# Kernel tuning notes

Measured on AMD Instinct MI355X. Metric: run time of the kernel, lower is better.

The kernel has to match this reference:

```python
import jax, jax.numpy as jnp
import numpy as np


def setup_inputs() -> dict:
    key = jax.random.key(0)
    k1, k2, k3 = jax.random.split(key, 3)
    B, L = 128, 4096           # batch, max document length
    O, W = 10, 5               # max options, max words per option
    V = 50000                  # vocab size for word indices
    document_indices = jax.random.randint(k1, (B, L), 0, V, dtype=jnp.int64)
    document_probabilities = jax.random.uniform(k2, (B, L), dtype=jnp.float32)
    options = jax.random.randint(k3, (B, O, W), 0, V, dtype=jnp.int64)
    return {
        "document_indices": document_indices,
        "document_probabilities": document_probabilities,
        "options": options,
    }


def reference(document_indices, document_probabilities, options):
    # match: (B, O, W, L) -- True where an option word equals a document word
    match = options[:, :, :, None] == document_indices[:, None, None, :]
    # per option-word probability: sum doc probabilities at matching positions
    word_probs = jnp.sum(
        jnp.where(match, document_probabilities[:, None, None, :], jnp.float32(0.0)),
        axis=3,
    )  # (B, O, W)
    sum_option_words = jnp.sum(word_probs, axis=2)  # (B, O)
    # multiword_option_mode == 'mean': divide by number of non-padding words
    divisor = jnp.sum((options != 0).astype(jnp.float32), axis=2)  # (B, O)
    return sum_option_words / divisor
```

## Files before the change

### kernel.cpp

```cpp
#include <hip/hip_runtime.h>

#define BB 128
#define LL 4096
#define OO 10
#define WW 5

__global__ __launch_bounds__(256) void OptionAttentionSum_kernel(
    const int* __restrict__ doc_idx,
    const float* __restrict__ doc_prob,
    const int* __restrict__ options,
    float* __restrict__ out)
{
    const int bo = blockIdx.x;
    const int b = bo / OO;
    const int t = threadIdx.x;

    const int* opt = options + bo * WW;
    const int w0 = opt[0], w1 = opt[1], w2 = opt[2], w3 = opt[3], w4 = opt[4];

    const int4*   idx4 = (const int4*)(doc_idx + (long)b * LL);
    const float4* p4   = (const float4*)(doc_prob + (long)b * LL);

    float acc = 0.0f;
#pragma unroll
    for (int it = 0; it < 4; ++it) {
        const int i = it * 256 + t;
        const int4   d = idx4[i];
        const float4 p = p4[i];
        acc += p.x * (float)((d.x == w0) + (d.x == w1) + (d.x == w2) + (d.x == w3) + (d.x == w4));
        acc += p.y * (float)((d.y == w0) + (d.y == w1) + (d.y == w2) + (d.y == w3) + (d.y == w4));
        acc += p.z * (float)((d.z == w0) + (d.z == w1) + (d.z == w2) + (d.z == w3) + (d.z == w4));
        acc += p.w * (float)((d.w == w0) + (d.w == w1) + (d.w == w2) + (d.w == w3) + (d.w == w4));
    }

#pragma unroll
    for (int off = 32; off > 0; off >>= 1)
        acc += __shfl_down(acc, off, 64);

    __shared__ float warp_sums[4];
    const int wave = t >> 6;
    const int lane = t & 63;
    if (lane == 0) warp_sums[wave] = acc;
    __syncthreads();

    if (t == 0) {
        const float total = warp_sums[0] + warp_sums[1] + warp_sums[2] + warp_sums[3];
        const float divisor = (float)((w0 != 0) + (w1 != 0) + (w2 != 0) + (w3 != 0) + (w4 != 0));
        out[bo] = total / divisor;
    }
}

extern "C" void kernel_launch(void* const* d_in, const int* in_sizes, int n_in,
                              void* d_out, int out_size, void* d_ws, size_t ws_size,
                              hipStream_t stream) {
    const int*   doc_idx  = (const int*)d_in[0];
    const float* doc_prob = (const float*)d_in[1];
    const int*   options  = (const int*)d_in[2];
    float*       out      = (float*)d_out;

    OptionAttentionSum_kernel<<<BB * OO, 256, 0, stream>>>(doc_idx, doc_prob, options, out);
}
```

Before: 64.46 us.

## Process all options per batch row in one block to reuse document loads

Each block now handles one batch row with 1024 threads, loading each document element once and testing it against all 10 options' 50 words, keeping 10 accumulators per thread. This removes the 10x redundant reads of the document indices and probabilities that the per-option blocks caused. In exchange, only 128 blocks are launched, so parallelism drops, register pressure rises, and there are ten wave reductions per block. Indexing w[0]+t*WW with a runtime t may push the word array into scratch memory.

```diff
diff --git a/kernel.cpp b/kernel.cpp
--- a/kernel.cpp
+++ b/kernel.cpp
@@ -5,48 +5,61 @@
 #define OO 10
 #define WW 5
 
-__global__ __launch_bounds__(256) void OptionAttentionSum_kernel(
+__global__ __launch_bounds__(1024) void OptionAttentionSum_kernel(
     const int* __restrict__ doc_idx,
     const float* __restrict__ doc_prob,
     const int* __restrict__ options,
     float* __restrict__ out)
 {
-    const int bo = blockIdx.x;
-    const int b = bo / OO;
+    const int b = blockIdx.x;
     const int t = threadIdx.x;
 
-    const int* opt = options + bo * WW;
-    const int w0 = opt[0], w1 = opt[1], w2 = opt[2], w3 = opt[3], w4 = opt[4];
+    const int* opt = options + b * (OO * WW);
+    int w[OO][WW];
+#pragma unroll
+    for (int o = 0; o < OO; ++o)
+#pragma unroll
+        for (int k = 0; k < WW; ++k)
+            w[o][k] = opt[o * WW + k];
 
-    const int4*   idx4 = (const int4*)(doc_idx + (long)b * LL);
-    const float4* p4   = (const float4*)(doc_prob + (long)b * LL);
+    const int4   d = ((const int4*)(doc_idx + (long)b * LL))[t];
+    const float4 p = ((const float4*)(doc_prob + (long)b * LL))[t];
 
-    float acc = 0.0f;
+    float acc[OO];
 #pragma unroll
-    for (int it = 0; it < 4; ++it) {
-        const int i = it * 256 + t;
-        const int4   d = idx4[i];
-        const float4 p = p4[i];
-        acc += p.x * (float)((d.x == w0) + (d.x == w1) + (d.x == w2) + (d.x == w3) + (d.x == w4));
-        acc += p.y * (float)((d.y == w0) + (d.y == w1) + (d.y == w2) + (d.y == w3) + (d.y == w4));
-        acc += p.z * (float)((d.z == w0) + (d.z == w1) + (d.z == w2) + (d.z == w3) + (d.z == w4));
-        acc += p.w * (float)((d.w == w0) + (d.w == w1) + (d.w == w2) + (d.w == w3) + (d.w == w4));
+    for (int o = 0; o < OO; ++o) acc[o] = 0.0f;
+
+#pragma unroll
+    for (int o = 0; o < OO; ++o) {
+        acc[o] += p.x * (float)((d.x == w[o][0]) + (d.x == w[o][1]) + (d.x == w[o][2]) + (d.x == w[o][3]) + (d.x == w[o][4]));
+        acc[o] += p.y * (float)((d.y == w[o][0]) + (d.y == w[o][1]) + (d.y == w[o][2]) + (d.y == w[o][3]) + (d.y == w[o][4]));
+        acc[o] += p.z * (float)((d.z == w[o][0]) + (d.z == w[o][1]) + (d.z == w[o][2]) + (d.z == w[o][3]) + (d.z == w[o][4]));
+        acc[o] += p.w * (float)((d.w == w[o][0]) + (d.w == w[o][1]) + (d.w == w[o][2]) + (d.w == w[o][3]) + (d.w == w[o][4]));
     }
 
 #pragma unroll
-    for (int off = 32; off > 0; off >>= 1)
-        acc += __shfl_down(acc, off, 64);
+    for (int o = 0; o < OO; ++o)
+#pragma unroll
+        for (int off = 32; off > 0; off >>= 1)
+            acc[o] += __shfl_down(acc[o], off, 64);
 
-    __shared__ float warp_sums[4];
+    __shared__ float wsum[16][OO];
     const int wave = t >> 6;
     const int lane = t & 63;
-    if (lane == 0) warp_sums[wave] = acc;
+    if (lane == 0) {
+#pragma unroll
+        for (int o = 0; o < OO; ++o) wsum[wave][o] = acc[o];
+    }
     __syncthreads();
 
-    if (t == 0) {
-        const float total = warp_sums[0] + warp_sums[1] + warp_sums[2] + warp_sums[3];
-        const float divisor = (float)((w0 != 0) + (w1 != 0) + (w2 != 0) + (w3 != 0) + (w4 != 0));
-        out[bo] = total / divisor;
+    if (t < OO) {
+        float total = 0.0f;
+#pragma unroll
+        for (int v = 0; v < 16; ++v) total += wsum[v][t];
+        const int* ow = w[0] + t * WW;
+        const float divisor = (float)((ow[0] != 0) + (ow[1] != 0) + (ow[2] != 0) +
+                                      (ow[3] != 0) + (ow[4] != 0));
+        out[b * OO + t] = total / divisor;
     }
 }
 
@@ -58,5 +71,5 @@
     const int*   options  = (const int*)d_in[2];
     float*       out      = (float*)d_out;
 
-    OptionAttentionSum_kernel<<<BB * OO, 256, 0, stream>>>(doc_idx, doc_prob, options, out);
+    OptionAttentionSum_kernel<<<BB, 1024, 0, stream>>>(doc_idx, doc_prob, options, out);
 }
```

Measured after the change: 67.66 us. 1.05x slower.

## Process two options per block to halve document reloads

Applied to the files above, without the earlier changes.

Each block now handles two options of the same batch row, so the document indices and probabilities are loaded once and compared against ten words instead of five. The grid shrinks from 1280 to 640 blocks, and blocks are ordered batch-minor so that neighbouring blocks read different documents. This cuts redundant global/L2 traffic, at the cost of less parallelism and more ALU work per thread.

```diff
diff --git a/kernel.cpp b/kernel.cpp
--- a/kernel.cpp
+++ b/kernel.cpp
@@ -11,42 +11,53 @@
     const int* __restrict__ options,
     float* __restrict__ out)
 {
-    const int bo = blockIdx.x;
-    const int b = bo / OO;
+    const int b    = blockIdx.x & (BB - 1);
+    const int pair = blockIdx.x >> 7;
+    const int o0 = pair * 2, o1 = pair * 2 + 1;
     const int t = threadIdx.x;
 
-    const int* opt = options + bo * WW;
-    const int w0 = opt[0], w1 = opt[1], w2 = opt[2], w3 = opt[3], w4 = opt[4];
+    const int* opt = options + (b * OO + o0) * WW;
+    const int a0 = opt[0], a1 = opt[1], a2 = opt[2], a3 = opt[3], a4 = opt[4];
+    const int b0 = opt[5], b1 = opt[6], b2 = opt[7], b3 = opt[8], b4 = opt[9];
 
     const int4*   idx4 = (const int4*)(doc_idx + (long)b * LL);
     const float4* p4   = (const float4*)(doc_prob + (long)b * LL);
 
-    float acc = 0.0f;
+    float accA = 0.0f, accB = 0.0f;
 #pragma unroll
     for (int it = 0; it < 4; ++it) {
         const int i = it * 256 + t;
         const int4   d = idx4[i];
         const float4 p = p4[i];
-        acc += p.x * (float)((d.x == w0) + (d.x == w1) + (d.x == w2) + (d.x == w3) + (d.x == w4));
-        acc += p.y * (float)((d.y == w0) + (d.y == w1) + (d.y == w2) + (d.y == w3) + (d.y == w4));
-        acc += p.z * (float)((d.z == w0) + (d.z == w1) + (d.z == w2) + (d.z == w3) + (d.z == w4));
-        acc += p.w * (float)((d.w == w0) + (d.w == w1) + (d.w == w2) + (d.w == w3) + (d.w == w4));
+        accA += p.x * (float)((d.x == a0) + (d.x == a1) + (d.x == a2) + (d.x == a3) + (d.x == a4));
+        accA += p.y * (float)((d.y == a0) + (d.y == a1) + (d.y == a2) + (d.y == a3) + (d.y == a4));
+        accA += p.z * (float)((d.z == a0) + (d.z == a1) + (d.z == a2) + (d.z == a3) + (d.z == a4));
+        accA += p.w * (float)((d.w == a0) + (d.w == a1) + (d.w == a2) + (d.w == a3) + (d.w == a4));
+        accB += p.x * (float)((d.x == b0) + (d.x == b1) + (d.x == b2) + (d.x == b3) + (d.x == b4));
+        accB += p.y * (float)((d.y == b0) + (d.y == b1) + (d.y == b2) + (d.y == b3) + (d.y == b4));
+        accB += p.z * (float)((d.z == b0) + (d.z == b1) + (d.z == b2) + (d.z == b3) + (d.z == b4));
+        accB += p.w * (float)((d.w == b0) + (d.w == b1) + (d.w == b2) + (d.w == b3) + (d.w == b4));
     }
 
 #pragma unroll
-    for (int off = 32; off > 0; off >>= 1)
-        acc += __shfl_down(acc, off, 64);
+    for (int off = 32; off > 0; off >>= 1) {
+        accA += __shfl_xor(accA, off, 64);
+        accB += __shfl_xor(accB, off, 64);
+    }
 
-    __shared__ float warp_sums[4];
+    __shared__ float wsumA[4], wsumB[4];
     const int wave = t >> 6;
     const int lane = t & 63;
-    if (lane == 0) warp_sums[wave] = acc;
+    if (lane == 0) { wsumA[wave] = accA; wsumB[wave] = accB; }
     __syncthreads();
 
     if (t == 0) {
-        const float total = warp_sums[0] + warp_sums[1] + warp_sums[2] + warp_sums[3];
-        const float divisor = (float)((w0 != 0) + (w1 != 0) + (w2 != 0) + (w3 != 0) + (w4 != 0));
-        out[bo] = total / divisor;
+        const float totA = wsumA[0] + wsumA[1] + wsumA[2] + wsumA[3];
+        const float totB = wsumB[0] + wsumB[1] + wsumB[2] + wsumB[3];
+        const float divA = (float)((a0 != 0) + (a1 != 0) + (a2 != 0) + (a3 != 0) + (a4 != 0));
+        const float divB = (float)((b0 != 0) + (b1 != 0) + (b2 != 0) + (b3 != 0) + (b4 != 0));
+        out[b * OO + o0] = totA / divA;
+        out[b * OO + o1] = totB / divB;
     }
 }
 
@@ -58,5 +69,5 @@
     const int*   options  = (const int*)d_in[2];
     float*       out      = (float*)d_out;
 
-    OptionAttentionSum_kernel<<<BB * OO, 256, 0, stream>>>(doc_idx, doc_prob, options, out);
+    OptionAttentionSum_kernel<<<BB * (OO / 2), 256, 0, stream>>>(doc_idx, doc_prob, options, out);
 }
```

Result: faster. 60.33 us (-6.4%).
